# Performance work log

Measured on AMD Instinct MI355X. Metric: run time of the kernel, lower is better.

Reference implementation:

```python
import jax, jax.numpy as jnp
import numpy as np

B, L, D, NUM_NODES = 256, 512, 128, 1024


def setup_inputs() -> dict:
    key = jax.random.key(0)
    k1, k2, k3, k4, k5, k6 = jax.random.split(key, 6)
    src_ids = jax.random.randint(k1, (B, L), 0, NUM_NODES, dtype=jnp.int32)
    dst_ids = jax.random.randint(k2, (B, L), 0, NUM_NODES, dtype=jnp.int32)
    s = 1.0  # nn.Linear default init is uniform; randn is fine for a numeric baseline
    W1 = jax.random.normal(k3, (1, D), dtype=jnp.float32) * s
    b1 = jax.random.normal(k4, (D,), dtype=jnp.float32) * 0.01
    W2 = jax.random.normal(k5, (D, D), dtype=jnp.float32) * (1.0 / np.sqrt(D))
    b2 = jax.random.normal(k6, (D,), dtype=jnp.float32) * 0.01
    return {"src_ids": src_ids, "dst_ids": dst_ids, "W1": W1, "b1": b1, "W2": W2, "b2": b2}


def _counts_in(a, b):
    # counts_in[i, j] = number of occurrences of a[i, j] within b[i, :]
    # matches np.unique counts / dict-lookup semantics (missing key -> 0)
    return (a[:, :, None] == b[:, None, :]).sum(axis=-1).astype(jnp.float32)


def _encode(appearances, W1, b1, W2, b2):
    # appearances: (B, L, 2) -> unsqueeze(-1) -> Linear(1, D) -> ReLU -> Linear(D, D) -> sum over the 2 count channels
    h = jax.nn.relu(appearances[..., None] * W1[0] + b1)      # (B, L, 2, D)
    h = jnp.einsum('blcd,de->blce', h, W2) + b2               # (B, L, 2, D)
    return h.sum(axis=2)                                      # (B, L, D)


def reference(src_ids, dst_ids, W1, b1, W2, b2):
    # co-occurrence appearance counts
    src_app = jnp.stack([_counts_in(src_ids, src_ids), _counts_in(src_ids, dst_ids)], axis=-1)  # (B, Ls, 2)
    dst_app = jnp.stack([_counts_in(dst_ids, src_ids), _counts_in(dst_ids, dst_ids)], axis=-1)  # (B, Ld, 2)
    # zero out padded positions (node id == 0)
    src_app = jnp.where(src_ids[..., None] == 0, 0.0, src_app)
    dst_app = jnp.where(dst_ids[..., None] == 0, 0.0, dst_app)
    src_feat = _encode(src_app, W1, b1, W2, b2)
    dst_feat = _encode(dst_app, W1, b1, W2, b2)
    return src_feat, dst_feat
```

## Files before the change

kernel.cpp:

```cpp
#include <hip/hip_runtime.h>


#define BB      256
#define LL      512
#define DD      128
#define NNODES  1024
#define CMAX    512
#define SPLITS  4
#define ROWS_PER (LL / SPLITS)

typedef float f4x __attribute__((ext_vector_type(4)));

__global__ __launch_bounds__(DD) void build_table_kernel(
    const float* __restrict__ W1, const float* __restrict__ b1,
    const float* __restrict__ W2, const float* __restrict__ b2,
    float* __restrict__ T) {
  const int c = blockIdx.x;
  const int e = threadIdx.x;
  __shared__ float h[DD];
  h[e] = fmaxf((float)c * W1[e] + b1[e], 0.0f);
  __syncthreads();
  float acc = b2[e];
#pragma unroll 16
  for (int d = 0; d < DD; ++d) acc = fmaf(h[d], W2[d * DD + e], acc);
  T[c * DD + e] = acc;
}

__global__ __launch_bounds__(256) void encode_kernel(
    const int* __restrict__ src_ids, const int* __restrict__ dst_ids,
    const float* __restrict__ T, float* __restrict__ out) {
  const int batch = blockIdx.x >> 2;
  const int split = blockIdx.x & (SPLITS - 1);
  const int tid   = threadIdx.x;

  __shared__ int hist[2 * NNODES];
  __shared__ int cnt[4 * ROWS_PER];

#pragma unroll
  for (int i = tid; i < 2 * NNODES; i += 256) hist[i] = 0;
  __syncthreads();

  const int* sb = src_ids + batch * LL;
  const int* db = dst_ids + batch * LL;
#pragma unroll
  for (int i = tid; i < LL; i += 256) {
    atomicAdd(&hist[sb[i]], 1);
    atomicAdd(&hist[NNODES + db[i]], 1);
  }
  __syncthreads();

  const int r0 = split * ROWS_PER;
  if (tid < ROWS_PER) {
    const int sid = sb[r0 + tid];
    const int did = db[r0 + tid];
    cnt[tid]                = sid ? hist[sid] : 0;
    cnt[ROWS_PER + tid]     = sid ? hist[NNODES + sid] : 0;
    cnt[2 * ROWS_PER + tid] = did ? hist[did] : 0;
    cnt[3 * ROWS_PER + tid] = did ? hist[NNODES + did] : 0;
  }
  __syncthreads();

  const int lane = tid & 31;
  const int rsub = tid >> 5;
  float* out_s = out + ((size_t)batch * LL + r0) * DD;
  float* out_d = out_s + (size_t)BB * LL * DD;

#pragma unroll 4
  for (int rr = rsub; rr < ROWS_PER; rr += 8) {
    const f4x a = ((const f4x*)(T + (size_t)cnt[rr] * DD))[lane];
    const f4x b = ((const f4x*)(T + (size_t)cnt[ROWS_PER + rr] * DD))[lane];
    const f4x c = ((const f4x*)(T + (size_t)cnt[2 * ROWS_PER + rr] * DD))[lane];
    const f4x d = ((const f4x*)(T + (size_t)cnt[3 * ROWS_PER + rr] * DD))[lane];
    const f4x vs = a + b;
    const f4x vd = c + d;
    __builtin_nontemporal_store(vs, ((f4x*)(out_s + (size_t)rr * DD)) + lane);
    __builtin_nontemporal_store(vd, ((f4x*)(out_d + (size_t)rr * DD)) + lane);
  }
}

extern "C" void kernel_launch(void* const* d_in, const int* in_sizes, int n_in,
                              void* d_out, int out_size, void* d_ws, size_t ws_size,
                              hipStream_t stream) {
  const int*   src = (const int*)d_in[0];
  const int*   dst = (const int*)d_in[1];
  const float* W1  = (const float*)d_in[2];
  const float* b1  = (const float*)d_in[3];
  const float* W2  = (const float*)d_in[4];
  const float* b2  = (const float*)d_in[5];
  float* out = (float*)d_out;
  float* T   = (float*)d_ws;

  build_table_kernel<<<CMAX + 1, DD, 0, stream>>>(W1, b1, W2, b2, T);
  encode_kernel<<<BB * SPLITS, 256, 0, stream>>>(src, dst, T, out);
}
```

Before: 157.7 us.

## Fuse table build into encode kernel, computing only needed count rows in LDS

Removes the separate kernel that built a 513-row lookup table in global memory. Each encode block now finds the distinct count values its rows use, compacts them into slots, and computes only those MLP rows into shared memory, reusing the histogram's shared buffer. The gathers then read from LDS instead of global memory. In exchange, every block redoes a small MLP with repeated W2 reads from cache before it can start its output stores. The code also assumes at most 64 distinct count values per block.

```diff
diff --git a/kernel.cpp b/kernel.cpp
--- a/kernel.cpp
+++ b/kernel.cpp
@@ -5,39 +5,34 @@
 #define LL      512
 #define DD      128
 #define NNODES  1024
-#define CMAX    512
 #define SPLITS  4
 #define ROWS_PER (LL / SPLITS)
+#define CMAXP1  (LL + 1)
+#define TBL_SLOTS 64
 
 typedef float f4x __attribute__((ext_vector_type(4)));
 
-__global__ __launch_bounds__(DD) void build_table_kernel(
+__global__ __launch_bounds__(256) void fused_encode_kernel(
+    const int* __restrict__ src_ids, const int* __restrict__ dst_ids,
     const float* __restrict__ W1, const float* __restrict__ b1,
     const float* __restrict__ W2, const float* __restrict__ b2,
-    float* __restrict__ T) {
-  const int c = blockIdx.x;
-  const int e = threadIdx.x;
-  __shared__ float h[DD];
-  h[e] = fmaxf((float)c * W1[e] + b1[e], 0.0f);
-  __syncthreads();
-  float acc = b2[e];
-#pragma unroll 16
-  for (int d = 0; d < DD; ++d) acc = fmaf(h[d], W2[d * DD + e], acc);
-  T[c * DD + e] = acc;
-}
+    float* __restrict__ out) {
+  __shared__ __align__(16) float tbl[TBL_SLOTS * DD];
+  __shared__ int slotOf[CMAXP1];
+  __shared__ int cnt[4 * ROWS_PER];
+  __shared__ int cOf[TBL_SLOTS];
+  __shared__ int ns;
 
-__global__ __launch_bounds__(256) void encode_kernel(
-    const int* __restrict__ src_ids, const int* __restrict__ dst_ids,
-    const float* __restrict__ T, float* __restrict__ out) {
+  int* hist = (int*)tbl;
+
   const int batch = blockIdx.x >> 2;
   const int split = blockIdx.x & (SPLITS - 1);
   const int tid   = threadIdx.x;
 
-  __shared__ int hist[2 * NNODES];
-  __shared__ int cnt[4 * ROWS_PER];
-
 #pragma unroll
   for (int i = tid; i < 2 * NNODES; i += 256) hist[i] = 0;
+  for (int i = tid; i < CMAXP1; i += 256) slotOf[i] = -1;
+  if (tid == 0) ns = 0;
   __syncthreads();
 
   const int* sb = src_ids + batch * LL;
@@ -50,13 +45,40 @@
   __syncthreads();
 
   const int r0 = split * ROWS_PER;
-  if (tid < ROWS_PER) {
-    const int sid = sb[r0 + tid];
-    const int did = db[r0 + tid];
-    cnt[tid]                = sid ? hist[sid] : 0;
-    cnt[ROWS_PER + tid]     = sid ? hist[NNODES + sid] : 0;
-    cnt[2 * ROWS_PER + tid] = did ? hist[did] : 0;
-    cnt[3 * ROWS_PER + tid] = did ? hist[NNODES + did] : 0;
+#pragma unroll
+  for (int i = tid; i < 4 * ROWS_PER; i += 256) {
+    const int r  = i & (ROWS_PER - 1);
+    const int g  = i >> 7;
+    const int id = (g < 2 ? sb : db)[r0 + r];
+    const int c  = id ? hist[(g & 1) * NNODES + id] : 0;
+    cnt[i] = c;
+    slotOf[c] = 1;
+  }
+  __syncthreads();
+
+  for (int c = tid; c < CMAXP1; c += 256) {
+    if (slotOf[c] >= 0) {
+      const int s = atomicAdd(&ns, 1);
+      slotOf[c] = s;
+      cOf[s] = c;
+    }
+  }
+  __syncthreads();
+
+#pragma unroll
+  for (int i = tid; i < 4 * ROWS_PER; i += 256) cnt[i] = slotOf[cnt[i]];
+
+  {
+    const int nslots = ns;
+    const int e = tid & (DD - 1);
+    for (int s = tid >> 7; s < nslots; s += 2) {
+      const float fc = (float)cOf[s];
+      float acc = b2[e];
+#pragma unroll 16
+      for (int d = 0; d < DD; ++d)
+        acc = fmaf(fmaxf(fmaf(fc, W1[d], b1[d]), 0.0f), W2[d * DD + e], acc);
+      tbl[s * DD + e] = acc;
+    }
   }
   __syncthreads();
 
@@ -64,17 +86,16 @@
   const int rsub = tid >> 5;
   float* out_s = out + ((size_t)batch * LL + r0) * DD;
   float* out_d = out_s + (size_t)BB * LL * DD;
+  const f4x* tb = (const f4x*)tbl;
 
 #pragma unroll 4
   for (int rr = rsub; rr < ROWS_PER; rr += 8) {
-    const f4x a = ((const f4x*)(T + (size_t)cnt[rr] * DD))[lane];
-    const f4x b = ((const f4x*)(T + (size_t)cnt[ROWS_PER + rr] * DD))[lane];
-    const f4x c = ((const f4x*)(T + (size_t)cnt[2 * ROWS_PER + rr] * DD))[lane];
-    const f4x d = ((const f4x*)(T + (size_t)cnt[3 * ROWS_PER + rr] * DD))[lane];
-    const f4x vs = a + b;
-    const f4x vd = c + d;
-    __builtin_nontemporal_store(vs, ((f4x*)(out_s + (size_t)rr * DD)) + lane);
-    __builtin_nontemporal_store(vd, ((f4x*)(out_d + (size_t)rr * DD)) + lane);
+    const f4x a = tb[cnt[rr] * (DD / 4) + lane];
+    const f4x b = tb[cnt[ROWS_PER + rr] * (DD / 4) + lane];
+    const f4x c = tb[cnt[2 * ROWS_PER + rr] * (DD / 4) + lane];
+    const f4x d = tb[cnt[3 * ROWS_PER + rr] * (DD / 4) + lane];
+    __builtin_nontemporal_store(a + b, ((f4x*)(out_s + (size_t)rr * DD)) + lane);
+    __builtin_nontemporal_store(c + d, ((f4x*)(out_d + (size_t)rr * DD)) + lane);
   }
 }
 
@@ -87,9 +108,6 @@
   const float* b1  = (const float*)d_in[3];
   const float* W2  = (const float*)d_in[4];
   const float* b2  = (const float*)d_in[5];
-  float* out = (float*)d_out;
-  float* T   = (float*)d_ws;
-
-  build_table_kernel<<<CMAX + 1, DD, 0, stream>>>(W1, b1, W2, b2, T);
-  encode_kernel<<<BB * SPLITS, 256, 0, stream>>>(src, dst, T, out);
+  fused_encode_kernel<<<BB * SPLITS, 256, 0, stream>>>(
+      src, dst, W1, b1, W2, b2, (float*)d_out);
 }
```

New measurement: 164.0 us. +4.0%, slower.
